# Kernel optimization log

Hardware: AMD Instinct MI355X
Metric: run time of the kernel (lower is better)

The kernel has to match this reference:

```python
import jax, jax.numpy as jnp
import numpy as np

# All gates (RY, CNOT) and the |0...0> initial state are real-valued, so the
# complex state vector of the original torchquantum circuit stays real; we
# simulate with float32 amplitudes and probs = state**2 == |state|**2.
# Wire convention matches torchquantum get_states_1d(): wire 0 is the most
# significant bit of the flattened state index.

N_BLOCKS = 4
N_QUBITS = 22


def setup_inputs() -> dict:
    key = jax.random.key(0)
    phi = jax.random.normal(key, (N_BLOCKS, N_QUBITS), dtype=jnp.float32) * 0.5
    return {"phi": phi}


def _apply_ry(state, theta, q, n_qubits):
    # RY(theta) = [[cos(t/2), -sin(t/2)], [sin(t/2), cos(t/2)]] on wire q
    dim = state.shape[0]
    pre = 2 ** q
    post = dim // (2 * pre)
    st = state.reshape(pre, 2, post)
    c = jnp.cos(theta * 0.5)
    s = jnp.sin(theta * 0.5)
    new = jnp.stack([c * st[:, 0] - s * st[:, 1],
                     s * st[:, 0] + c * st[:, 1]], axis=1)
    return new.reshape(dim)


def _apply_cnot(state, q, n_qubits):
    # CNOT with control=q, target=q+1 (adjacent wires): flip target when control=1
    dim = state.shape[0]
    pre = 2 ** q
    post = dim // (4 * pre)
    st = state.reshape(pre, 2, 2, post)
    st = jnp.concatenate([st[:, :1], st[:, 1:, ::-1]], axis=1)
    return st.reshape(dim)


def reference(phi):
    n_blocks, n_qubits = phi.shape
    dim = 2 ** n_qubits
    state = jnp.zeros((dim,), dtype=phi.dtype).at[0].set(1.0)  # |0...0>
    for b in range(n_blocks):
        for q in range(n_qubits):
            state = _apply_ry(state, phi[b, q], q, n_qubits)
        for q in range(n_qubits - 1):
            state = _apply_cnot(state, q, n_qubits)
    probs = state * state  # |amplitude|^2, state is real
    return probs
```

## Files before the change

kernel.cpp:

```cpp
#include <hip/hip_runtime.h>
#include <math.h>


#define VPRE_OFF 0
#define WSUF_OFF 16384
#define CS_OFF   32768

__device__ __forceinline__ float ry_el(float c, float s, int o, int i) {
  return (o == 0) ? ((i == 0) ? c : -s) : ((i == 0) ? s : c);
}

__device__ __forceinline__ void build_M(const float* __restrict__ ws, int w, int jb,
                                        float* __restrict__ Mm) {
  const float c0 = ws[CS_OFF + w],      s0 = ws[CS_OFF + 88 + w];
  const float c1 = ws[CS_OFF + 22 + w], s1 = ws[CS_OFF + 88 + 22 + w];
  const float c2 = ws[CS_OFF + 44 + w], s2 = ws[CS_OFF + 88 + 44 + w];
  const float c3 = ws[CS_OFF + 66 + w], s3 = ws[CS_OFF + 88 + 66 + w];
  #pragma unroll
  for (int o = 0; o < 8; ++o) {
    const int Xp = (o >> 2) & 1, Yp = (o >> 1) & 1, Zp = o & 1;
    const float r3 = ry_el(c3, s3, jb, Xp);
    #pragma unroll
    for (int i = 0; i < 8; ++i) {
      const int X = (i >> 2) & 1, Y = (i >> 1) & 1, Z = i & 1;
      const float r2 = ry_el(c2, s2, X ^ Xp, Yp);
      const float r1 = ry_el(c1, s1, Y ^ Yp, Zp);
      const float f0 = ((Z ^ Zp) == 0) ? c0 : s0;
      Mm[o * 8 + i] = r3 * r2 * r1 * f0;
    }
  }
}

__global__ __launch_bounds__(256) void qc_build_tables(const float* __restrict__ phi,
                                                       float* __restrict__ ws) {
  __shared__ float bufA[8192];
  __shared__ float bufB[8192];
  const int tid = threadIdx.x;

  if (tid < 88) {
    const float t = 0.5f * phi[tid];
    ws[CS_OFF + tid]      = cosf(t);
    ws[CS_OFF + 88 + tid] = sinf(t);
  }
  __threadfence();
  __syncthreads();

  float* cur = bufA;
  float* nxt = bufB;

  if (blockIdx.x == 0) {
    if (tid == 0) {
      #pragma unroll
      for (int r = 0; r < 8; ++r) cur[r] = (r == 0) ? 1.0f : 0.0f;
    }
    __syncthreads();
    int size = 1;
    for (int w = 0; w <= 10; ++w) {
      const int jb = tid & 1;
      float Mm[64];
      build_M(ws, w, jb, Mm);
      const int newsize = size << 1;
      for (int t = tid; t < newsize; t += 256) {
        const float* v = cur + (t >> 1) * 8;
        float inv[8], outv[8];
        #pragma unroll
        for (int i = 0; i < 8; ++i) inv[i] = v[i];
        #pragma unroll
        for (int o = 0; o < 8; ++o) {
          float acc = 0.0f;
          #pragma unroll
          for (int i = 0; i < 8; ++i) acc += Mm[o * 8 + i] * inv[i];
          outv[o] = acc;
        }
        if (w == 10) {
          #pragma unroll
          for (int o = 0; o < 8; ++o) ws[VPRE_OFF + t * 8 + o] = outv[o];
        } else {
          #pragma unroll
          for (int o = 0; o < 8; ++o) nxt[t * 8 + o] = outv[o];
        }
      }
      __syncthreads();
      float* tmp = cur; cur = nxt; nxt = tmp;
      size = newsize;
    }
  } else {
    if (tid == 0) {
      #pragma unroll
      for (int r = 0; r < 8; ++r) cur[r] = 1.0f;
    }
    __syncthreads();
    int size = 1;
    for (int w = 21; w >= 11; --w) {
      const int nb = 21 - w;
      const int newsize = size << 1;
      const int C = (newsize > 256) ? (newsize >> 8) : 1;
      const int jb = (newsize <= 256) ? ((tid >> nb) & 1) : ((tid >> 7) & 1);
      float Mm[64];
      build_M(ws, w, jb, Mm);
      for (int k = 0; k < C; ++k) {
        const int t = tid * C + k;
        if (t >= newsize) break;
        const int tp = t & ((1 << nb) - 1);
        const float* v = cur + tp * 8;
        float inv[8], outv[8];
        #pragma unroll
        for (int i = 0; i < 8; ++i) inv[i] = v[i];
        #pragma unroll
        for (int i = 0; i < 8; ++i) {
          float acc = 0.0f;
          #pragma unroll
          for (int o = 0; o < 8; ++o) acc += inv[o] * Mm[o * 8 + i];
          outv[i] = acc;
        }
        if (w == 11) {
          #pragma unroll
          for (int i = 0; i < 8; ++i) ws[WSUF_OFF + i * 2048 + t] = outv[i];
        } else {
          #pragma unroll
          for (int i = 0; i < 8; ++i) nxt[t * 8 + i] = outv[i];
        }
      }
      __syncthreads();
      float* tmp = cur; cur = nxt; nxt = tmp;
      size = newsize;
    }
  }
}

__global__ __launch_bounds__(256) void qc_finalize(const float* __restrict__ ws,
                                                   float* __restrict__ out) {
  __shared__ float lw[16384];
  const int tid = threadIdx.x;
  {
    const float4* src = (const float4*)(ws + WSUF_OFF);
    float4* dst = (float4*)lw;
    #pragma unroll
    for (int i = 0; i < 16; ++i) dst[tid + i * 256] = src[tid + i * 256];
  }
  __syncthreads();

  #pragma unroll
  for (int sg = 0; sg < 4; ++sg) {
    const unsigned seg  = blockIdx.x * 4u + sg;
    const unsigned base = seg << 11;
    const unsigned p    = (base ^ (base >> 1)) >> 11;
    const float* vp = ws + VPRE_OFF + p * 8;
    const float v0 = vp[0], v1 = vp[1], v2 = vp[2], v3 = vp[3];
    const float v4 = vp[4], v5 = vp[5], v6 = vp[6], v7 = vp[7];
    #pragma unroll
    for (int k = 0; k < 8; ++k) {
      const unsigned I = base + (unsigned)(k * 256) + tid;
      const unsigned J = I ^ (I >> 1);
      const unsigned s = J & 2047u;
      const float acc = lw[s]            * v0 + lw[2048 + s]     * v1
                      + lw[2 * 2048 + s] * v2 + lw[3 * 2048 + s] * v3
                      + lw[4 * 2048 + s] * v4 + lw[5 * 2048 + s] * v5
                      + lw[6 * 2048 + s] * v6 + lw[7 * 2048 + s] * v7;
      out[I] = acc * acc;
    }
  }
}

extern "C" void kernel_launch(void* const* d_in, const int* in_sizes, int n_in,
                              void* d_out, int out_size, void* d_ws, size_t ws_size,
                              hipStream_t stream) {
  (void)in_sizes; (void)n_in; (void)out_size; (void)ws_size;
  const float* phi = (const float*)d_in[0];
  float* out = (float*)d_out;
  float* ws  = (float*)d_ws;

  qc_build_tables<<<2, 256, 0, stream>>>(phi, ws);
  qc_finalize<<<512, 256, 0, stream>>>(ws, out);
}
```

Before: 77.36 us.

## Compute prefix/suffix tables per-thread in parallel across 16 blocks

The table-building kernel no longer grows prefix and suffix vectors level by level in shared memory with barriers on only two blocks. Instead, each of 4096 threads independently computes its own 8-vector by walking its bit path through 11 wires. It also replaces the dense 8x8 matrix build with a factored sequence of 2x2 rotations. This removes the serial dependency chain, the syncs and the 64-element per-thread matrices in exchange for redundant per-thread work.

```diff
diff --git a/kernel.cpp b/kernel.cpp
--- a/kernel.cpp
+++ b/kernel.cpp
@@ -4,127 +4,116 @@
 
 #define VPRE_OFF 0
 #define WSUF_OFF 16384
-#define CS_OFF   32768
 
-__device__ __forceinline__ float ry_el(float c, float s, int o, int i) {
-  return (o == 0) ? ((i == 0) ? c : -s) : ((i == 0) ? s : c);
+__device__ __forceinline__ void apply_col(float v[8],
+    float c0, float s0, float c1, float s1,
+    float c2, float s2, float c3, float s3, int jb) {
+  float a[8], b[8], t[8];
+  #pragma unroll
+  for (int xy = 0; xy < 4; ++xy) {
+    const float v0 = v[xy * 2 + 0], v1 = v[xy * 2 + 1];
+    a[xy * 2 + 0] = c0 * v0 + s0 * v1;
+    a[xy * 2 + 1] = s0 * v0 + c0 * v1;
+  }
+  #pragma unroll
+  for (int X = 0; X < 2; ++X) {
+    #pragma unroll
+    for (int Zp = 0; Zp < 2; ++Zp) {
+      const float a0 = a[X * 4 + 0 + Zp], a1 = a[X * 4 + 2 + Zp];
+      const float r10 = Zp ? -s1 : c1;
+      const float r11 = Zp ?  c1 : s1;
+      b[X * 4 + 0 + Zp] = r10 * a0 + r11 * a1;
+      b[X * 4 + 2 + Zp] = r11 * a0 + r10 * a1;
+    }
+  }
+  #pragma unroll
+  for (int Yp = 0; Yp < 2; ++Yp) {
+    #pragma unroll
+    for (int Zp = 0; Zp < 2; ++Zp) {
+      const float b0 = b[0 + Yp * 2 + Zp], b1 = b[4 + Yp * 2 + Zp];
+      const float r20 = Yp ? -s2 : c2;
+      const float r21 = Yp ?  c2 : s2;
+      t[0 + Yp * 2 + Zp] = r20 * b0 + r21 * b1;
+      t[4 + Yp * 2 + Zp] = r21 * b0 + r20 * b1;
+    }
+  }
+  const float m0 = jb ? s3 : c3;
+  const float m1 = jb ? c3 : -s3;
+  #pragma unroll
+  for (int yz = 0; yz < 4; ++yz) { v[yz] = m0 * t[yz]; v[4 + yz] = m1 * t[4 + yz]; }
 }
 
-__device__ __forceinline__ void build_M(const float* __restrict__ ws, int w, int jb,
-                                        float* __restrict__ Mm) {
-  const float c0 = ws[CS_OFF + w],      s0 = ws[CS_OFF + 88 + w];
-  const float c1 = ws[CS_OFF + 22 + w], s1 = ws[CS_OFF + 88 + 22 + w];
-  const float c2 = ws[CS_OFF + 44 + w], s2 = ws[CS_OFF + 88 + 44 + w];
-  const float c3 = ws[CS_OFF + 66 + w], s3 = ws[CS_OFF + 88 + 66 + w];
+__device__ __forceinline__ void apply_row(float r[8],
+    float c0, float s0, float c1, float s1,
+    float c2, float s2, float c3, float s3, int jb) {
+  float g[8], h[8], k[8];
+  const float m0 = jb ? s3 : c3;
+  const float m1 = jb ? c3 : -s3;
   #pragma unroll
-  for (int o = 0; o < 8; ++o) {
-    const int Xp = (o >> 2) & 1, Yp = (o >> 1) & 1, Zp = o & 1;
-    const float r3 = ry_el(c3, s3, jb, Xp);
+  for (int yz = 0; yz < 4; ++yz) { g[yz] = m0 * r[yz]; g[4 + yz] = m1 * r[4 + yz]; }
+  #pragma unroll
+  for (int Yp = 0; Yp < 2; ++Yp) {
     #pragma unroll
-    for (int i = 0; i < 8; ++i) {
-      const int X = (i >> 2) & 1, Y = (i >> 1) & 1, Z = i & 1;
-      const float r2 = ry_el(c2, s2, X ^ Xp, Yp);
-      const float r1 = ry_el(c1, s1, Y ^ Yp, Zp);
-      const float f0 = ((Z ^ Zp) == 0) ? c0 : s0;
-      Mm[o * 8 + i] = r3 * r2 * r1 * f0;
+    for (int Zp = 0; Zp < 2; ++Zp) {
+      const float g0 = g[0 + Yp * 2 + Zp], g1 = g[4 + Yp * 2 + Zp];
+      const float r20 = Yp ? -s2 : c2;
+      const float r21 = Yp ?  c2 : s2;
+      h[0 + Yp * 2 + Zp] = g0 * r20 + g1 * r21;
+      h[4 + Yp * 2 + Zp] = g0 * r21 + g1 * r20;
     }
+  }
+  #pragma unroll
+  for (int X = 0; X < 2; ++X) {
+    #pragma unroll
+    for (int Zp = 0; Zp < 2; ++Zp) {
+      const float h0 = h[X * 4 + 0 + Zp], h1 = h[X * 4 + 2 + Zp];
+      const float r10 = Zp ? -s1 : c1;
+      const float r11 = Zp ?  c1 : s1;
+      k[X * 4 + 0 + Zp] = h0 * r10 + h1 * r11;
+      k[X * 4 + 2 + Zp] = h0 * r11 + h1 * r10;
+    }
+  }
+  #pragma unroll
+  for (int xy = 0; xy < 4; ++xy) {
+    const float k0 = k[xy * 2 + 0], k1 = k[xy * 2 + 1];
+    r[xy * 2 + 0] = k0 * c0 + k1 * s0;
+    r[xy * 2 + 1] = k0 * s0 + k1 * c0;
   }
 }
 
-__global__ __launch_bounds__(256) void qc_build_tables(const float* __restrict__ phi,
-                                                       float* __restrict__ ws) {
-  __shared__ float bufA[8192];
-  __shared__ float bufB[8192];
+__global__ __launch_bounds__(256) void qc_build(const float* __restrict__ phi,
+                                                float* __restrict__ ws) {
+  __shared__ float cs[176];
   const int tid = threadIdx.x;
-
   if (tid < 88) {
     const float t = 0.5f * phi[tid];
-    ws[CS_OFF + tid]      = cosf(t);
-    ws[CS_OFF + 88 + tid] = sinf(t);
+    cs[tid]      = cosf(t);
+    cs[88 + tid] = sinf(t);
   }
-  __threadfence();
   __syncthreads();
-
-  float* cur = bufA;
-  float* nxt = bufB;
-
-  if (blockIdx.x == 0) {
-    if (tid == 0) {
-      #pragma unroll
-      for (int r = 0; r < 8; ++r) cur[r] = (r == 0) ? 1.0f : 0.0f;
+  const int bid = blockIdx.x;
+  if (bid < 8) {
+    const int t = bid * 256 + tid;
+    float v[8] = {1.f, 0.f, 0.f, 0.f, 0.f, 0.f, 0.f, 0.f};
+    #pragma unroll
+    for (int w = 0; w <= 10; ++w) {
+      const int jb = (t >> (10 - w)) & 1;
+      apply_col(v, cs[w], cs[88 + w], cs[22 + w], cs[110 + w],
+                cs[44 + w], cs[132 + w], cs[66 + w], cs[154 + w], jb);
     }
-    __syncthreads();
-    int size = 1;
-    for (int w = 0; w <= 10; ++w) {
-      const int jb = tid & 1;
-      float Mm[64];
-      build_M(ws, w, jb, Mm);
-      const int newsize = size << 1;
-      for (int t = tid; t < newsize; t += 256) {
-        const float* v = cur + (t >> 1) * 8;
-        float inv[8], outv[8];
-        #pragma unroll
-        for (int i = 0; i < 8; ++i) inv[i] = v[i];
-        #pragma unroll
-        for (int o = 0; o < 8; ++o) {
-          float acc = 0.0f;
-          #pragma unroll
-          for (int i = 0; i < 8; ++i) acc += Mm[o * 8 + i] * inv[i];
-          outv[o] = acc;
-        }
-        if (w == 10) {
-          #pragma unroll
-          for (int o = 0; o < 8; ++o) ws[VPRE_OFF + t * 8 + o] = outv[o];
-        } else {
-          #pragma unroll
-          for (int o = 0; o < 8; ++o) nxt[t * 8 + o] = outv[o];
-        }
-      }
-      __syncthreads();
-      float* tmp = cur; cur = nxt; nxt = tmp;
-      size = newsize;
+    #pragma unroll
+    for (int o = 0; o < 8; ++o) ws[VPRE_OFF + t * 8 + o] = v[o];
+  } else {
+    const int t = (bid - 8) * 256 + tid;
+    float r[8] = {1.f, 1.f, 1.f, 1.f, 1.f, 1.f, 1.f, 1.f};
+    #pragma unroll
+    for (int w = 21; w >= 11; --w) {
+      const int jb = (t >> (21 - w)) & 1;
+      apply_row(r, cs[w], cs[88 + w], cs[22 + w], cs[110 + w],
+                cs[44 + w], cs[132 + w], cs[66 + w], cs[154 + w], jb);
     }
-  } else {
-    if (tid == 0) {
-      #pragma unroll
-      for (int r = 0; r < 8; ++r) cur[r] = 1.0f;
-    }
-    __syncthreads();
-    int size = 1;
-    for (int w = 21; w >= 11; --w) {
-      const int nb = 21 - w;
-      const int newsize = size << 1;
-      const int C = (newsize > 256) ? (newsize >> 8) : 1;
-      const int jb = (newsize <= 256) ? ((tid >> nb) & 1) : ((tid >> 7) & 1);
-      float Mm[64];
-      build_M(ws, w, jb, Mm);
-      for (int k = 0; k < C; ++k) {
-        const int t = tid * C + k;
-        if (t >= newsize) break;
-        const int tp = t & ((1 << nb) - 1);
-        const float* v = cur + tp * 8;
-        float inv[8], outv[8];
-        #pragma unroll
-        for (int i = 0; i < 8; ++i) inv[i] = v[i];
-        #pragma unroll
-        for (int i = 0; i < 8; ++i) {
-          float acc = 0.0f;
-          #pragma unroll
-          for (int o = 0; o < 8; ++o) acc += inv[o] * Mm[o * 8 + i];
-          outv[i] = acc;
-        }
-        if (w == 11) {
-          #pragma unroll
-          for (int i = 0; i < 8; ++i) ws[WSUF_OFF + i * 2048 + t] = outv[i];
-        } else {
-          #pragma unroll
-          for (int i = 0; i < 8; ++i) nxt[t * 8 + i] = outv[i];
-        }
-      }
-      __syncthreads();
-      float* tmp = cur; cur = nxt; nxt = tmp;
-      size = newsize;
-    }
+    #pragma unroll
+    for (int i = 0; i < 8; ++i) ws[WSUF_OFF + i * 2048 + t] = r[i];
   }
 }
 
@@ -170,6 +159,6 @@
   float* out = (float*)d_out;
   float* ws  = (float*)d_ws;
 
-  qc_build_tables<<<2, 256, 0, stream>>>(phi, ws);
+  qc_build<<<16, 256, 0, stream>>>(phi, ws);
   qc_finalize<<<512, 256, 0, stream>>>(ws, out);
 }
```

Result: faster. 65.27 us (-15.6%).
